# Optimization experiments

Hardware: AMD Instinct MI355X
Metric: run time of the kernel (lower is better)

Reference implementation:

```python
import jax, jax.numpy as jnp
import numpy as np

ITER_ROUTING = 3          # cfg.iter_routing default in CapsNet repo
EPS = 1e-7                # tf.keras.backend.epsilon()
NUM_CAPS_IN = 1152
IN_DIM = 8
OUT_DIM = 16


def _squash(s):
    # s: [..., vec_len]; squash along the vector dimension (axis=-2 of the
    # original [B,1,16,1] layout == last axis here)
    sq = jnp.sum(s * s, axis=-1, keepdims=True)
    return (sq / (1.0 + sq)) * s / (jnp.sqrt(sq) + EPS)


def _routing(x, W, num_outputs):
    # x: [B, K, 8]  primary capsules; W: [J, K, 8, 16] per-output-capsule weights
    # u_hat[j,b,k,u] = sum_d W[j,k,d,u] * x[b,k,d]   (matmul with transpose_a)
    u_hat = jnp.einsum('jkdu,bkd->jbku', W, x)  # [J, B, K, 16]
    K = x.shape[1]
    b_IJ = jnp.zeros((K, num_outputs), dtype=x.dtype)  # logits shared across batch
    vs = []
    for j in range(num_outputs):            # sequential per original: b_IJ carries over
        uh = u_hat[j]                        # [B, K, 16]
        v = None
        for _ in range(ITER_ROUTING):
            c = jax.nn.softmax(b_IJ, axis=1)            # [K, J]
            s = jnp.einsum('k,bku->bu', c[:, j], uh)    # weighted sum over input caps
            v = _squash(s)                               # [B, 16]
            # agreement: sum over batch and vec dims of <u_hat, v>
            agree = jnp.einsum('bku,bu->k', uh, v)       # [K]
            b_IJ = b_IJ.at[:, j].add(agree)
        vs.append(v)
    # concat along capsule axis -> [B, J, 16, 1]
    return jnp.stack(vs, axis=1)[..., None]


def setup_inputs() -> dict:
    key = jax.random.key(0)
    k1, k2 = jax.random.split(key)
    B = 512
    inputs = jax.random.normal(k1, (B, NUM_CAPS_IN, IN_DIM, 1), dtype=jnp.float32)
    # original: np.random.normal(scale=0.01), one W per output capsule j
    W = 0.01 * jax.random.normal(k2, (10, NUM_CAPS_IN, IN_DIM, OUT_DIM), dtype=jnp.float32)
    return {"inputs": inputs, "W": W, "num_outputs": 10}


def reference(inputs, W, num_outputs):
    x = inputs[..., 0]  # [B, 1152, 8]
    return _routing(x, W, num_outputs)
```

## Files before the change

### kernel.cpp

```cpp
#include <hip/hip_runtime.h>

typedef unsigned int uint;
typedef unsigned short ushort_t;

#define NB 512
#define NK 1152
#define ND 8
#define NU 16
#define NJ 10
#define NPH 30
#define EPSQ 1e-7f

#define KT 36
#define KCN 32
#define BT 16
#define BGN 32
#define XPH 296
#define WPH 136
#define SREDP 20
#define SVP 20

#define OFF_BL 0
#define OFF_P  11520
#define OFF_XB (OFF_P + KCN*NB*NU)
#define OFF_WTB (OFF_XB + (NB*NK*ND)/2)

__device__ __forceinline__ ushort_t b16(float f) {
  uint u = __float_as_uint(f);
  return (ushort_t)((u + 0x7fffu + ((u >> 16) & 1u)) >> 16);
}
__device__ __forceinline__ void up8(const uint4 v, float* f) {
  f[0] = __uint_as_float(v.x << 16); f[1] = __uint_as_float(v.x & 0xffff0000u);
  f[2] = __uint_as_float(v.y << 16); f[3] = __uint_as_float(v.y & 0xffff0000u);
  f[4] = __uint_as_float(v.z << 16); f[5] = __uint_as_float(v.z & 0xffff0000u);
  f[6] = __uint_as_float(v.w << 16); f[7] = __uint_as_float(v.w & 0xffff0000u);
}
__device__ __forceinline__ float dot8(const float* a, const float* b) {
  return a[0]*b[0] + a[1]*b[1] + a[2]*b[2] + a[3]*b[3] +
         a[4]*b[4] + a[5]*b[5] + a[6]*b[6] + a[7]*b[7];
}

__global__ __launch_bounds__(256) void caps_init(const float* __restrict__ x,
                                                 const float* __restrict__ W,
                                                 float* __restrict__ bl,
                                                 ushort_t* __restrict__ Xb,
                                                 ushort_t* __restrict__ WTb) {
  const int g = blockIdx.x * 256 + threadIdx.x;
  if (g < NK * NJ) bl[g] = 0.f;
  if (g < (NB * NK * ND) / 8) {
    const float4* xp = (const float4*)x + (size_t)g * 2;
    const float4 a = xp[0], b = xp[1];
    uint4 o;
    o.x = (uint)b16(a.x) | ((uint)b16(a.y) << 16);
    o.y = (uint)b16(a.z) | ((uint)b16(a.w) << 16);
    o.z = (uint)b16(b.x) | ((uint)b16(b.y) << 16);
    o.w = (uint)b16(b.z) | ((uint)b16(b.w) << 16);
    ((uint4*)Xb)[g] = o;
  }
  if (g < (NJ * NK * NU * ND) / 8) {
    const int u = g & 15;
    const int k = (g >> 4) % NK;
    const int j = g / (NK * NU);
    const float* wp = W + ((size_t)(j * NK + k) * ND) * NU + u;
    uint4 o;
    o.x = (uint)b16(wp[0])  | ((uint)b16(wp[16]) << 16);
    o.y = (uint)b16(wp[32]) | ((uint)b16(wp[48]) << 16);
    o.z = (uint)b16(wp[64]) | ((uint)b16(wp[80]) << 16);
    o.w = (uint)b16(wp[96]) | ((uint)b16(wp[112]) << 16);
    ((uint4*)WTb)[g] = o;
  }
}

__global__ __launch_bounds__(256, 4) void caps_part(
    const ushort_t* __restrict__ Xb, const ushort_t* __restrict__ WTb,
    const float* __restrict__ bl, float* __restrict__ partial, int js) {
  __shared__ __align__(16) ushort_t sxu[BT * XPH];
  __shared__ __align__(16) ushort_t swu[KT * WPH];
  __shared__ float sc[KT];
  float* sred = (float*)sxu;
  const int tid = threadIdx.x;
  const int kc = blockIdx.x & (KCN - 1);
  const int bgi = blockIdx.x >> 5;
  const int b0 = bgi * BT;
  const int k0 = kc * KT;

  {
    const uint4* gx = (const uint4*)Xb + ((size_t)b0 * NK + k0);
    for (int i = tid; i < BT * KT; i += 256) {
      const int b = i / KT, q = i - b * KT;
      *(uint4*)&sxu[b * XPH + q * 8] = gx[(size_t)b * NK + q];
    }
  }
  {
    const uint4* gw = (const uint4*)WTb + ((size_t)js * NK + k0) * NU;
    for (int i = tid; i < KT * NU; i += 256) {
      const int k = i >> 4, u = i & 15;
      *(uint4*)&swu[k * WPH + u * 8] = gw[i];
    }
  }
  if (tid < KT) {
    const float* row = bl + (size_t)(k0 + tid) * NJ;
    float r[NJ];
#pragma unroll
    for (int jj = 0; jj < NJ; ++jj) r[jj] = row[jj];
    float mx = r[0];
#pragma unroll
    for (int jj = 1; jj < NJ; ++jj) mx = fmaxf(mx, r[jj]);
    float se = 0.f;
#pragma unroll
    for (int jj = 0; jj < NJ; ++jj) se += __expf(r[jj] - mx);
    sc[tid] = __expf(r[js] - mx) / se;
  }
  __syncthreads();

  const int w = tid >> 6;
  const int lane = tid & 63;
  const int kq = lane >> 4;
  const int bq = (lane >> 2) & 3;
  const int uq = lane & 3;
  float a[4][4];
#pragma unroll
  for (int i = 0; i < 4; ++i)
#pragma unroll
    for (int m = 0; m < 4; ++m) a[i][m] = 0.f;

#pragma unroll
  for (int it = 0; it < 3; ++it) {
    const int kli = it * 4 + kq;
    if (kli < 9) {
      const int kl = w * 9 + kli;
      const float ck = sc[kl];
      float xd[4][8];
#pragma unroll
      for (int i = 0; i < 4; ++i)
        up8(*(const uint4*)&sxu[(bq * 4 + i) * XPH + kl * 8], xd[i]);
#pragma unroll
      for (int m = 0; m < 4; ++m) {
        float wd[8];
        up8(*(const uint4*)&swu[kl * WPH + (uq * 4 + m) * 8], wd);
#pragma unroll
        for (int i = 0; i < 4; ++i)
          a[i][m] = fmaf(ck, dot8(xd[i], wd), a[i][m]);
      }
    }
  }
#pragma unroll
  for (int i = 0; i < 4; ++i)
#pragma unroll
    for (int m = 0; m < 4; ++m) {
      a[i][m] += __shfl_xor(a[i][m], 16, 64);
      a[i][m] += __shfl_xor(a[i][m], 32, 64);
    }
  __syncthreads();
  if (kq == 0) {
#pragma unroll
    for (int i = 0; i < 4; ++i) {
      const float4 t4 = {a[i][0], a[i][1], a[i][2], a[i][3]};
      *(float4*)&sred[(w * BT + bq * 4 + i) * SREDP + uq * 4] = t4;
    }
  }
  __syncthreads();
  {
    const int b = tid >> 4, u = tid & 15;
    const float sv =
        sred[(0 * BT + b) * SREDP + u] + sred[(1 * BT + b) * SREDP + u] +
        sred[(2 * BT + b) * SREDP + u] + sred[(3 * BT + b) * SREDP + u];
    partial[(size_t)kc * (NB * NU) + (size_t)(b0 + b) * NU + u] = sv;
  }
}

__global__ __launch_bounds__(256, 4) void caps_agp(
    const ushort_t* __restrict__ Xb, const ushort_t* __restrict__ WTb,
    const float* __restrict__ partial, float* __restrict__ bl,
    float* __restrict__ out, int ja, int wout) {
  __shared__ __align__(16) ushort_t sxu[BT * XPH];
  __shared__ __align__(16) ushort_t swu[KT * WPH];
  __shared__ float sv[BT * SVP];
  const int tid = threadIdx.x;
  const int kc = blockIdx.x & (KCN - 1);
  const int bgi = blockIdx.x >> 5;
  const int b0 = bgi * BT;
  const int k0 = kc * KT;

  {
    const uint4* gx = (const uint4*)Xb + ((size_t)b0 * NK + k0);
    for (int i = tid; i < BT * KT; i += 256) {
      const int b = i / KT, q = i - b * KT;
      *(uint4*)&sxu[b * XPH + q * 8] = gx[(size_t)b * NK + q];
    }
  }
  {
    const uint4* gw = (const uint4*)WTb + ((size_t)ja * NK + k0) * NU;
    for (int i = tid; i < KT * NU; i += 256) {
      const int k = i >> 4, u = i & 15;
      *(uint4*)&swu[k * WPH + u * 8] = gw[i];
    }
  }
  {
    const int b = tid >> 4, u = tid & 15;
    const float* pp = partial + (size_t)(b0 + b) * NU + u;
    float s = 0.f;
#pragma unroll
    for (int c = 0; c < KCN; ++c) s += pp[(size_t)c * (NB * NU)];
    float sq = s * s;
    sq += __shfl_xor(sq, 1, 64);
    sq += __shfl_xor(sq, 2, 64);
    sq += __shfl_xor(sq, 4, 64);
    sq += __shfl_xor(sq, 8, 64);
    const float scale = (sq / (1.f + sq)) / (sqrtf(sq) + EPSQ);
    const float vv = scale * s;
    sv[b * SVP + u] = vv;
    if (wout && kc == 0) out[((size_t)(b0 + b) * NJ + ja) * NU + u] = vv;
  }
  __syncthreads();

  const int w = tid >> 6;
  const int lane = tid & 63;
  const int kq = lane >> 4;
  const int bq = (lane >> 2) & 3;
  const int uq = lane & 3;
  float4 vf[4];
#pragma unroll
  for (int i = 0; i < 4; ++i)
    vf[i] = *(const float4*)&sv[(bq * 4 + i) * SVP + uq * 4];

#pragma unroll
  for (int it = 0; it < 3; ++it) {
    const int kli = it * 4 + kq;
    if (kli < 9) {
      const int kl = w * 9 + kli;
      float xd[4][8];
#pragma unroll
      for (int i = 0; i < 4; ++i)
        up8(*(const uint4*)&sxu[(bq * 4 + i) * XPH + kl * 8], xd[i]);
      float ag = 0.f;
#pragma unroll
      for (int m = 0; m < 4; ++m) {
        float wd[8];
        up8(*(const uint4*)&swu[kl * WPH + (uq * 4 + m) * 8], wd);
#pragma unroll
        for (int i = 0; i < 4; ++i) {
          const float vm = (m == 0) ? vf[i].x
                         : (m == 1) ? vf[i].y
                         : (m == 2) ? vf[i].z : vf[i].w;
          ag = fmaf(vm, dot8(xd[i], wd), ag);
        }
      }
      ag += __shfl_xor(ag, 1, 64);
      ag += __shfl_xor(ag, 2, 64);
      ag += __shfl_xor(ag, 4, 64);
      ag += __shfl_xor(ag, 8, 64);
      if ((lane & 15) == 0)
        atomicAdd(&bl[(size_t)(k0 + kl) * NJ + ja], ag);
    }
  }
}

__global__ __launch_bounds__(256) void caps_finout(const float* __restrict__ partial,
                                                   float* __restrict__ out) {
  const int g = blockIdx.x * 256 + threadIdx.x;
  const int b = g >> 4, u = g & 15;
  float s = 0.f;
#pragma unroll
  for (int c = 0; c < KCN; ++c)
    s += partial[(size_t)c * (NB * NU) + (size_t)b * NU + u];
  float sq = s * s;
  sq += __shfl_xor(sq, 1, 64);
  sq += __shfl_xor(sq, 2, 64);
  sq += __shfl_xor(sq, 4, 64);
  sq += __shfl_xor(sq, 8, 64);
  const float scale = (sq / (1.f + sq)) / (sqrtf(sq) + EPSQ);
  out[((size_t)b * NJ + (NJ - 1)) * NU + u] = scale * s;
}

extern "C" void kernel_launch(void* const* d_in, const int* in_sizes, int n_in,
                              void* d_out, int out_size, void* d_ws,
                              size_t ws_size, hipStream_t stream) {
  (void)in_sizes; (void)n_in; (void)out_size; (void)ws_size;
  const float* x = (const float*)d_in[0];
  const float* W = (const float*)d_in[1];
  float* out = (float*)d_out;
  float* ws = (float*)d_ws;
  float* bl = ws + OFF_BL;
  float* pt = ws + OFF_P;
  ushort_t* Xb  = (ushort_t*)(ws + OFF_XB);
  ushort_t* WTb = (ushort_t*)(ws + OFF_WTB);

  caps_init<<<(NB * NK * ND / 8 + 255) / 256, 256, 0, stream>>>(x, W, bl, Xb,
                                                                WTb);
  for (int n = 0; n < NPH; ++n) {
    const int j = n / 3, t = n - 3 * j;
    if (n > 0) {
      const int ja = (t == 0) ? (j - 1) : j;
      caps_agp<<<KCN * BGN, 256, 0, stream>>>(Xb, WTb, pt, bl, out, ja,
                                              (t == 0) ? 1 : 0);
    }
    caps_part<<<KCN * BGN, 256, 0, stream>>>(Xb, WTb, bl, pt, j);
  }
  caps_finout<<<(NB * NU) / 256, 256, 0, stream>>>(pt, out);
}
```

Before: 552.8 us.

## Replace per-chunk partial sums with atomic s accumulation and deterministic agreement partials

caps_part now atomically accumulates s into a per-phase buffer, so caps_agp and caps_finout read one value instead of summing 32 chunk partials. The agreement atomics on the logits are replaced by per-batch-group partial writes, which the next caps_part reduces while ping-ponging between two logit buffers. This is meant to cut global reads of the partial buffer and avoid contended atomics on the logits. In exchange it adds atomic float adds on s, which make the summation order nondeterministic, plus 32 extra loads per k row for the agreement reduction.

```diff
diff --git a/kernel.cpp b/kernel.cpp
--- a/kernel.cpp
+++ b/kernel.cpp
@@ -20,9 +20,11 @@
 #define SREDP 20
 #define SVP 20
 
-#define OFF_BL 0
-#define OFF_P  11520
-#define OFF_XB (OFF_P + KCN*NB*NU)
+#define OFF_BLA 0
+#define OFF_BLB (NK*NJ)
+#define OFF_AGP (2*NK*NJ)
+#define OFF_S   (OFF_AGP + NK*BGN)
+#define OFF_XB  (OFF_S + NPH*NB*NU)
 #define OFF_WTB (OFF_XB + (NB*NK*ND)/2)
 
 __device__ __forceinline__ ushort_t b16(float f) {
@@ -42,11 +44,13 @@
 
 __global__ __launch_bounds__(256) void caps_init(const float* __restrict__ x,
                                                  const float* __restrict__ W,
-                                                 float* __restrict__ bl,
+                                                 float* __restrict__ blA,
+                                                 float* __restrict__ s,
                                                  ushort_t* __restrict__ Xb,
                                                  ushort_t* __restrict__ WTb) {
   const int g = blockIdx.x * 256 + threadIdx.x;
-  if (g < NK * NJ) bl[g] = 0.f;
+  if (g < NK * NJ) blA[g] = 0.f;
+  if (g < NPH * NB * NU) s[g] = 0.f;
   if (g < (NB * NK * ND) / 8) {
     const float4* xp = (const float4*)x + (size_t)g * 2;
     const float4 a = xp[0], b = xp[1];
@@ -73,7 +77,9 @@
 
 __global__ __launch_bounds__(256, 4) void caps_part(
     const ushort_t* __restrict__ Xb, const ushort_t* __restrict__ WTb,
-    const float* __restrict__ bl, float* __restrict__ partial, int js) {
+    const float* __restrict__ blIn, float* __restrict__ blOut,
+    const float* __restrict__ agp_p, float* __restrict__ sn, int js,
+    int jaPrev) {
   __shared__ __align__(16) ushort_t sxu[BT * XPH];
   __shared__ __align__(16) ushort_t swu[KT * WPH];
   __shared__ float sc[KT];
@@ -99,10 +105,26 @@
     }
   }
   if (tid < KT) {
-    const float* row = bl + (size_t)(k0 + tid) * NJ;
+    const int k = k0 + tid;
+    const float* rowIn = blIn + (size_t)k * NJ;
     float r[NJ];
 #pragma unroll
-    for (int jj = 0; jj < NJ; ++jj) r[jj] = row[jj];
+    for (int jj = 0; jj < NJ; ++jj) r[jj] = rowIn[jj];
+    if (jaPrev >= 0) {
+      const float4* ap = (const float4*)(agp_p + (size_t)k * BGN);
+      float agsum = 0.f;
+#pragma unroll
+      for (int i = 0; i < BGN / 4; ++i) {
+        const float4 t4 = ap[i];
+        agsum += t4.x + t4.y + t4.z + t4.w;
+      }
+      r[jaPrev] += agsum;
+    }
+    if (bgi == 0) {
+      float* rowOut = blOut + (size_t)k * NJ;
+#pragma unroll
+      for (int jj = 0; jj < NJ; ++jj) rowOut[jj] = r[jj];
+    }
     float mx = r[0];
 #pragma unroll
     for (int jj = 1; jj < NJ; ++jj) mx = fmaxf(mx, r[jj]);
@@ -165,13 +187,13 @@
     const float sv =
         sred[(0 * BT + b) * SREDP + u] + sred[(1 * BT + b) * SREDP + u] +
         sred[(2 * BT + b) * SREDP + u] + sred[(3 * BT + b) * SREDP + u];
-    partial[(size_t)kc * (NB * NU) + (size_t)(b0 + b) * NU + u] = sv;
+    atomicAdd(&sn[(size_t)(b0 + b) * NU + u], sv);
   }
 }
 
 __global__ __launch_bounds__(256, 4) void caps_agp(
     const ushort_t* __restrict__ Xb, const ushort_t* __restrict__ WTb,
-    const float* __restrict__ partial, float* __restrict__ bl,
+    const float* __restrict__ sprev, float* __restrict__ agp_p,
     float* __restrict__ out, int ja, int wout) {
   __shared__ __align__(16) ushort_t sxu[BT * XPH];
   __shared__ __align__(16) ushort_t swu[KT * WPH];
@@ -198,10 +220,7 @@
   }
   {
     const int b = tid >> 4, u = tid & 15;
-    const float* pp = partial + (size_t)(b0 + b) * NU + u;
-    float s = 0.f;
-#pragma unroll
-    for (int c = 0; c < KCN; ++c) s += pp[(size_t)c * (NB * NU)];
+    const float s = sprev[(size_t)(b0 + b) * NU + u];
     float sq = s * s;
     sq += __shfl_xor(sq, 1, 64);
     sq += __shfl_xor(sq, 2, 64);
@@ -251,19 +270,16 @@
       ag += __shfl_xor(ag, 4, 64);
       ag += __shfl_xor(ag, 8, 64);
       if ((lane & 15) == 0)
-        atomicAdd(&bl[(size_t)(k0 + kl) * NJ + ja], ag);
-    }
-  }
-}
-
-__global__ __launch_bounds__(256) void caps_finout(const float* __restrict__ partial,
+        agp_p[(size_t)(k0 + kl) * BGN + bgi] = ag;
+    }
+  }
+}
+
+__global__ __launch_bounds__(256) void caps_finout(const float* __restrict__ slast,
                                                    float* __restrict__ out) {
   const int g = blockIdx.x * 256 + threadIdx.x;
   const int b = g >> 4, u = g & 15;
-  float s = 0.f;
-#pragma unroll
-  for (int c = 0; c < KCN; ++c)
-    s += partial[(size_t)c * (NB * NU) + (size_t)b * NU + u];
+  const float s = slast[(size_t)b * NU + u];
   float sq = s * s;
   sq += __shfl_xor(sq, 1, 64);
   sq += __shfl_xor(sq, 2, 64);
@@ -281,21 +297,28 @@
   const float* W = (const float*)d_in[1];
   float* out = (float*)d_out;
   float* ws = (float*)d_ws;
-  float* bl = ws + OFF_BL;
-  float* pt = ws + OFF_P;
+  float* blA = ws + OFF_BLA;
+  float* blB = ws + OFF_BLB;
+  float* agp = ws + OFF_AGP;
+  float* s   = ws + OFF_S;
   ushort_t* Xb  = (ushort_t*)(ws + OFF_XB);
   ushort_t* WTb = (ushort_t*)(ws + OFF_WTB);
 
-  caps_init<<<(NB * NK * ND / 8 + 255) / 256, 256, 0, stream>>>(x, W, bl, Xb,
-                                                                WTb);
+  caps_init<<<(NB * NK * ND / 8 + 255) / 256, 256, 0, stream>>>(x, W, blA, s,
+                                                                Xb, WTb);
   for (int n = 0; n < NPH; ++n) {
     const int j = n / 3, t = n - 3 * j;
-    if (n > 0) {
-      const int ja = (t == 0) ? (j - 1) : j;
-      caps_agp<<<KCN * BGN, 256, 0, stream>>>(Xb, WTb, pt, bl, out, ja,
-                                              (t == 0) ? 1 : 0);
-    }
-    caps_part<<<KCN * BGN, 256, 0, stream>>>(Xb, WTb, bl, pt, j);
-  }
-  caps_finout<<<(NB * NU) / 256, 256, 0, stream>>>(pt, out);
-}
+    const int ja = (t == 0) ? (j - 1) : j;
+    if (n > 0)
+      caps_agp<<<KCN * BGN, 256, 0, stream>>>(
+          Xb, WTb, s + (size_t)(n - 1) * NB * NU, agp, out, ja,
+          (t == 0) ? 1 : 0);
+    float* bin  = (n & 1) ? blB : blA;
+    float* bout = (n & 1) ? blA : blB;
+    caps_part<<<KCN * BGN, 256, 0, stream>>>(Xb, WTb, bin, bout, agp,
+                                             s + (size_t)n * NB * NU, j,
+                                             (n > 0) ? ja : -1);
+  }
+  caps_finout<<<(NB * NU) / 256, 256, 0, stream>>>(
+      s + (size_t)(NPH - 1) * NB * NU, out);
+}
```

Measured after the change: 519.4 us. 1.06x faster.
